# Kernel tuning notes

Hardware: AMD Instinct MI355X
Metric: run time of the kernel (lower is better)

The kernel has to match this reference:

```python
import jax, jax.numpy as jnp
import numpy as np

D_MODEL = 1024
NUM_HEADS = 16
HEAD_DIM = D_MODEL // NUM_HEADS  # 64
# NOTE: the original module passes scale=attention_head_size, so scores are
# MULTIPLIED by head_dim (64), not divided by sqrt(head_dim). Faithful quirk.
SCALE = float(HEAD_DIM)


def setup_inputs() -> dict:
    key = jax.random.key(0)
    ks = jax.random.split(key, 6)
    bs, s, d = 2, 2048, D_MODEL
    q = jax.random.normal(ks[0], (bs, s, d), dtype=jnp.float32)
    k = jax.random.normal(ks[1], (bs, s, d), dtype=jnp.float32)
    v = jax.random.normal(ks[2], (bs, s, d), dtype=jnp.float32)
    # nn.Linear weights, shape (out, in); no bias (qkv_bias=False)
    init = 1.0 / np.sqrt(d)
    Wq = jax.random.uniform(ks[3], (d, d), jnp.float32, -init, init)
    Wk = jax.random.uniform(ks[4], (d, d), jnp.float32, -init, init)
    Wv = jax.random.uniform(ks[5], (d, d), jnp.float32, -init, init)
    return {"q": q, "k": k, "v": v, "Wq": Wq, "Wk": Wk, "Wv": Wv}


def _split_heads(x):
    bs, s, _ = x.shape
    return x.reshape(bs, s, NUM_HEADS, HEAD_DIM).transpose(0, 2, 1, 3)  # bhsd


def reference(q, k, v, Wq, Wk, Wv):
    bs, s, d = q.shape
    qh = _split_heads(q @ Wq.T)  # [b,h,s,hd]
    kh = _split_heads(k @ Wk.T)
    vh = _split_heads(v @ Wv.T)
    sims = jnp.einsum('bhqd,bhkd->bhqk', qh, kh) * SCALE
    attn = jax.nn.softmax(sims, axis=-1)
    out = jnp.einsum('bhqk,bhkd->bhqd', attn, vh)  # [b,h,s,hd]
    out = out.transpose(0, 2, 1, 3).reshape(bs, s, d)
    return out
```

## Files before the change

### kernel.cpp

```cpp
#include <hip/hip_runtime.h>


typedef _Float16 half4 __attribute__((ext_vector_type(4)));
typedef _Float16 half8 __attribute__((ext_vector_type(8)));
typedef float floatx4 __attribute__((ext_vector_type(4)));

#define MFMA_F16(a, b, c) __builtin_amdgcn_mfma_f32_16x16x32_f16((a), (b), (c), 0, 0, 0)

constexpr int SEQ = 2048;
constexpr int DM = 1024;
constexpr int NH = 16;
constexpr int HD = 64;
constexpr float QSCALE = 92.33248261689366f;

__device__ __forceinline__ void gl2lds16(const _Float16* g, _Float16* l) {
  __builtin_amdgcn_global_load_lds(
      (const __attribute__((address_space(1))) void*)g,
      (__attribute__((address_space(3))) void*)l, 16, 0, 0);
}

__device__ inline void split4(const float4 f, half4& h, half4& l) {
  h[0] = (_Float16)f.x; l[0] = (_Float16)(f.x - (float)h[0]);
  h[1] = (_Float16)f.y; l[1] = (_Float16)(f.y - (float)h[1]);
  h[2] = (_Float16)f.z; l[2] = (_Float16)(f.z - (float)h[2]);
  h[3] = (_Float16)f.w; l[3] = (_Float16)(f.w - (float)h[3]);
}

__global__ __launch_bounds__(256) void convert_all(
    const float* __restrict__ q, const float* __restrict__ k,
    const float* __restrict__ v, const float* __restrict__ Wq,
    const float* __restrict__ Wk, const float* __restrict__ Wv,
    _Float16* __restrict__ xq_h, _Float16* __restrict__ xq_l,
    _Float16* __restrict__ xk_h, _Float16* __restrict__ xk_l,
    _Float16* __restrict__ xv_h,
    _Float16* __restrict__ Wqh, _Float16* __restrict__ Wql,
    _Float16* __restrict__ Wkh, _Float16* __restrict__ Wkl,
    _Float16* __restrict__ Wvh)
{
  const int bid = blockIdx.x;
  const float* src; _Float16* dh; _Float16* dl; int do_lo, i0;
  if (bid < 4096)       { src = q;  dh = xq_h; dl = xq_l; do_lo = 1; i0 = bid; }
  else if (bid < 8192)  { src = k;  dh = xk_h; dl = xk_l; do_lo = 1; i0 = bid - 4096; }
  else if (bid < 12288) { src = v;  dh = xv_h; dl = xv_h; do_lo = 0; i0 = bid - 8192; }
  else if (bid < 13312) { src = Wq; dh = Wqh;  dl = Wql;  do_lo = 1; i0 = bid - 12288; }
  else if (bid < 14336) { src = Wk; dh = Wkh;  dl = Wkl;  do_lo = 1; i0 = bid - 13312; }
  else                  { src = Wv; dh = Wvh;  dl = Wvh;  do_lo = 0; i0 = bid - 14336; }
  const int idx = i0 * 256 + threadIdx.x;
  float4 f = ((const float4*)src)[idx];
  half4 h, l; split4(f, h, l);
  *(half4*)(dh + (size_t)idx * 4) = h;
  if (do_lo) *(half4*)(dl + (size_t)idx * 4) = l;
}

__global__ __launch_bounds__(256, 1) void proj3_kernel(
    const _Float16* __restrict__ xq_h, const _Float16* __restrict__ xq_l,
    const _Float16* __restrict__ xk_h, const _Float16* __restrict__ xk_l,
    const _Float16* __restrict__ xv_h,
    const _Float16* __restrict__ Wqh, const _Float16* __restrict__ Wql,
    const _Float16* __restrict__ Wkh, const _Float16* __restrict__ Wkl,
    const _Float16* __restrict__ Wvh,
    _Float16* __restrict__ qh_hi, _Float16* __restrict__ qh_lo,
    _Float16* __restrict__ kh_hi, _Float16* __restrict__ kh_lo,
    _Float16* __restrict__ vh)
{
  __shared__ __align__(16) _Float16 Ahs[128][64];
  __shared__ __align__(16) _Float16 Als[128][64];
  __shared__ __align__(16) _Float16 Bhs[128][64];
  __shared__ __align__(16) _Float16 Bls[128][64];

  const int z = blockIdx.z;
  const _Float16 *Ahg, *Alg, *Bhg, *Blg;
  _Float16 *yh, *yl;
  float scale; int three;
  if (z == 0)      { Ahg = xq_h; Alg = xq_l; Bhg = Wqh; Blg = Wql;
                     yh = qh_hi; yl = qh_lo; scale = QSCALE; three = 1; }
  else if (z == 1) { Ahg = xk_h; Alg = xk_l; Bhg = Wkh; Blg = Wkl;
                     yh = kh_hi; yl = kh_lo; scale = 1.0f; three = 1; }
  else             { Ahg = xv_h; Alg = xv_h; Bhg = Wvh; Blg = Wvh;
                     yh = vh;    yl = vh;    scale = 1.0f; three = 0; }

  const int tid = threadIdx.x;
  const int bm = blockIdx.x;
  const int bn = blockIdx.y;
  const int lane = tid & 63, l15 = lane & 15, quad = lane >> 4;
  const int w = tid >> 6, wm = w >> 1, wn = w & 1;

  const int r8 = lane >> 3;
  const int cp8 = (((lane & 7) ^ r8)) * 8;
  int grow[4]; _Float16* la[4]; _Float16* lal[4]; _Float16* lb[4]; _Float16* lbl[4];
  #pragma unroll
  for (int i = 0; i < 4; i++) {
    const int g = w * 4 + i;
    grow[i] = g * 8 + r8;
    la[i]  = &Ahs[0][0] + g * 512;
    lal[i] = &Als[0][0] + g * 512;
    lb[i]  = &Bhs[0][0] + g * 512;
    lbl[i] = &Bls[0][0] + g * 512;
  }

  floatx4 acc[4][4];
  #pragma unroll
  for (int mt = 0; mt < 4; mt++)
    #pragma unroll
    for (int nt = 0; nt < 4; nt++)
      acc[mt][nt] = (floatx4){0.f, 0.f, 0.f, 0.f};

  for (int kk = 0; kk < DM; kk += 64) {
    __syncthreads();
    #pragma unroll
    for (int i = 0; i < 4; i++) {
      const size_t ga = (size_t)(bm * 128 + grow[i]) * DM + kk + cp8;
      const size_t gb = (size_t)(bn * 128 + grow[i]) * DM + kk + cp8;
      gl2lds16(Ahg + ga, la[i]);
      gl2lds16(Bhg + gb, lb[i]);
      if (three) {
        gl2lds16(Alg + ga, lal[i]);
        gl2lds16(Blg + gb, lbl[i]);
      }
    }
    __syncthreads();

    #pragma unroll
    for (int kc = 0; kc < 2; kc++) {
      const int swz = ((kc * 4 + quad) ^ (l15 & 7)) * 8;
      half8 ah[4], bh_[4], al[4], bl[4];
      #pragma unroll
      for (int t = 0; t < 4; t++) {
        ah[t]  = *(const half8*)&Ahs[wm * 64 + t * 16 + l15][swz];
        bh_[t] = *(const half8*)&Bhs[wn * 64 + t * 16 + l15][swz];
        if (three) {
          al[t] = *(const half8*)&Als[wm * 64 + t * 16 + l15][swz];
          bl[t] = *(const half8*)&Bls[wn * 64 + t * 16 + l15][swz];
        }
      }
      if (three) {
        #pragma unroll
        for (int mt = 0; mt < 4; mt++)
          #pragma unroll
          for (int nt = 0; nt < 4; nt++) {
            floatx4 t0 = MFMA_F16(ah[mt], bh_[nt], acc[mt][nt]);
            t0 = MFMA_F16(ah[mt], bl[nt], t0);
            acc[mt][nt] = MFMA_F16(al[mt], bh_[nt], t0);
          }
      } else {
        #pragma unroll
        for (int mt = 0; mt < 4; mt++)
          #pragma unroll
          for (int nt = 0; nt < 4; nt++)
            acc[mt][nt] = MFMA_F16(ah[mt], bh_[nt], acc[mt][nt]);
      }
    }
  }

  #pragma unroll
  for (int mt = 0; mt < 4; mt++)
    #pragma unroll
    for (int nt = 0; nt < 4; nt++)
      #pragma unroll
      for (int r = 0; r < 4; r++) {
        int gm = bm * 128 + wm * 64 + mt * 16 + quad * 4 + r;
        int gn = bn * 128 + wn * 64 + nt * 16 + l15;
        int b = gm >> 11, s = gm & 2047;
        int h = gn >> 6, d = gn & 63;
        size_t idx = ((size_t)(b * NH + h) * SEQ + s) * HD + d;
        float val = acc[mt][nt][r] * scale;
        _Float16 hi = (_Float16)val;
        yh[idx] = hi;
        if (three) yl[idx] = (_Float16)(val - (float)hi);
      }
}

__global__ __launch_bounds__(256) void transpose_v(const _Float16* __restrict__ vh,
                                                   _Float16* __restrict__ vhT)
{
  __shared__ __align__(16) _Float16 T[128][72];
  const int bh = blockIdx.x, sc = blockIdx.y, tid = threadIdx.x;
  const _Float16* src = vh + ((size_t)bh * SEQ + sc * 128) * HD;
  #pragma unroll
  for (int i = 0; i < 4; i++) {
    int c = i * 256 + tid, row = c >> 3, off = (c & 7) * 8;
    *(half8*)&T[row][off] = *(const half8*)(src + (size_t)row * HD + off);
  }
  __syncthreads();
  _Float16* dst = vhT + (size_t)bh * HD * SEQ + sc * 128;
  #pragma unroll
  for (int i = 0; i < 4; i++) {
    int c = i * 256 + tid, hd = c >> 4, off = (c & 15) * 8;
    int base32 = off & ~31, qsel = (off >> 3) & 3;
    half8 vv;
    #pragma unroll
    for (int j = 0; j < 8; j++) {
      int s_local = base32 + 16 * (j >> 2) + 4 * qsel + (j & 3);
      vv[j] = T[s_local][hd];
    }
    *(half8*)(dst + (size_t)hd * SEQ + off) = vv;
  }
}

__global__ __launch_bounds__(256, 4) void flash_kernel(
    const _Float16* __restrict__ qh_hi, const _Float16* __restrict__ qh_lo,
    const _Float16* __restrict__ kh_hi, const _Float16* __restrict__ kh_lo,
    const _Float16* __restrict__ vhT, float* __restrict__ Op, float2* __restrict__ ml)
{
  __shared__ __align__(16) _Float16 Kh[2][64][64];
  __shared__ __align__(16) _Float16 Kl[2][64][64];
  __shared__ __align__(16) _Float16 Vt[64][64];

  const int id = blockIdx.x;
  const int seq_ = id >> 3;
  const int bh = (id & 7) + 8 * (seq_ & 3);
  const int rem = seq_ >> 2;
  const int qb = rem & 15;
  const int kh = rem >> 4;
  const int tid = threadIdx.x;
  const int wq = tid >> 6;
  const int lane = tid & 63, l15 = lane & 15, quad = lane >> 4;

  const size_t bh_off = (size_t)bh * SEQ * HD;
  const _Float16* __restrict__ kh_p = kh_hi + bh_off;
  const _Float16* __restrict__ kl_p = kh_lo + bh_off;
  const _Float16* __restrict__ vt_p = vhT + (size_t)bh * HD * SEQ;
  const int qrow0 = qb * 128 + wq * 32;

  half8 bqh[2][2], bql[2][2];
  #pragma unroll
  for (int g = 0; g < 2; g++) {
    const _Float16* qp_h = qh_hi + bh_off + (size_t)(qrow0 + g * 16 + l15) * HD;
    const _Float16* qp_l = qh_lo + bh_off + (size_t)(qrow0 + g * 16 + l15) * HD;
    #pragma unroll
    for (int kc = 0; kc < 2; kc++) {
      bqh[g][kc] = *(const half8*)(qp_h + kc * 32 + quad * 8);
      bql[g][kc] = *(const half8*)(qp_l + kc * 32 + quad * 8);
    }
  }

  const int r8 = lane >> 3;
  const int cp8 = ((lane & 7) ^ r8) * 8;

  float m_[2] = {-3.0e38f, -3.0e38f};
  float l_[2] = {0.f, 0.f};
  floatx4 Oacc[2][4];
  #pragma unroll
  for (int g = 0; g < 2; g++)
    #pragma unroll
    for (int nd = 0; nd < 4; nd++) Oacc[g][nd] = (floatx4){0.f, 0.f, 0.f, 0.f};

  const int kt0 = kh * 16;
  {
    const int kbase = kt0 * 64;
    #pragma unroll
    for (int i = 0; i < 2; i++) {
      const int g = wq * 2 + i;
      const int r = g * 8 + r8;
      gl2lds16(kh_p + (size_t)(kbase + r) * HD + cp8, &Kh[0][0][0] + g * 512);
      gl2lds16(kl_p + (size_t)(kbase + r) * HD + cp8, &Kl[0][0][0] + g * 512);
    }
  }

  for (int kt = kt0; kt < kt0 + 16; kt++) {
    const int cur = kt & 1;
    const int kbase = kt * 64;
    __syncthreads();

    #pragma unroll
    for (int i = 0; i < 2; i++) {
      const int g = wq * 2 + i;
      const int r = g * 8 + r8;
      gl2lds16(vt_p + (size_t)r * SEQ + kbase + cp8, &Vt[0][0] + g * 512);
    }
    if (kt + 1 < kt0 + 16) {
      const int kb2 = (kt + 1) * 64, nxt = cur ^ 1;
      #pragma unroll
      for (int i = 0; i < 2; i++) {
        const int g = wq * 2 + i;
        const int r = g * 8 + r8;
        gl2lds16(kh_p + (size_t)(kb2 + r) * HD + cp8, &Kh[nxt][0][0] + g * 512);
        gl2lds16(kl_p + (size_t)(kb2 + r) * HD + cp8, &Kl[nxt][0][0] + g * 512);
      }
    }

    floatx4 sacc[2][4];
    const int r7 = l15 & 7;
    __builtin_amdgcn_s_setprio(1);
    #pragma unroll
    for (int nt = 0; nt < 4; nt++) {
      half8 akh0 = *(const half8*)&Kh[cur][nt * 16 + l15][((0 * 4 + quad) ^ r7) * 8];
      half8 akh1 = *(const half8*)&Kh[cur][nt * 16 + l15][((1 * 4 + quad) ^ r7) * 8];
      half8 akl0 = *(const half8*)&Kl[cur][nt * 16 + l15][((0 * 4 + quad) ^ r7) * 8];
      half8 akl1 = *(const half8*)&Kl[cur][nt * 16 + l15][((1 * 4 + quad) ^ r7) * 8];
      #pragma unroll
      for (int g = 0; g < 2; g++) {
        floatx4 s4 = (floatx4){0.f, 0.f, 0.f, 0.f};
        s4 = MFMA_F16(akh0, bqh[g][0], s4);
        s4 = MFMA_F16(akh1, bqh[g][1], s4);
        s4 = MFMA_F16(akh0, bql[g][0], s4);
        s4 = MFMA_F16(akh1, bql[g][1], s4);
        s4 = MFMA_F16(akl0, bqh[g][0], s4);
        s4 = MFMA_F16(akl1, bqh[g][1], s4);
        sacc[g][nt] = s4;
      }
    }
    __builtin_amdgcn_s_setprio(0);

    float alpha2[2];
    half8 bp8g[2][2];
    #pragma unroll
    for (int g = 0; g < 2; g++) {
      float rmax = sacc[g][0][0];
      #pragma unroll
      for (int nt = 0; nt < 4; nt++)
        #pragma unroll
        for (int r = 0; r < 4; r++) rmax = fmaxf(rmax, sacc[g][nt][r]);
      rmax = fmaxf(rmax, __shfl_xor(rmax, 16, 64));
      rmax = fmaxf(rmax, __shfl_xor(rmax, 32, 64));
      const float mnew = fmaxf(m_[g], rmax);
      alpha2[g] = exp2f(m_[g] - mnew);
      m_[g] = mnew;

      float rsum = 0.f;
      #pragma unroll
      for (int nt = 0; nt < 4; nt++)
        #pragma unroll
        for (int r = 0; r < 4; r++) {
          float p = exp2f(sacc[g][nt][r] - mnew);
          sacc[g][nt][r] = p;
          rsum += p;
        }
      rsum += __shfl_xor(rsum, 16, 64);
      rsum += __shfl_xor(rsum, 32, 64);
      l_[g] = l_[g] * alpha2[g] + rsum;

      #pragma unroll
      for (int kc = 0; kc < 2; kc++)
        #pragma unroll
        for (int j = 0; j < 8; j++)
          bp8g[g][kc][j] = (_Float16)sacc[g][2 * kc + (j >> 2)][j & 3];
    }

    __syncthreads();

    half8 av[4][2];
    #pragma unroll
    for (int nd = 0; nd < 4; nd++) {
      av[nd][0] = *(const half8*)&Vt[nd * 16 + l15][((0 * 4 + quad) ^ r7) * 8];
      av[nd][1] = *(const half8*)&Vt[nd * 16 + l15][((1 * 4 + quad) ^ r7) * 8];
    }

    __builtin_amdgcn_s_setprio(1);
    #pragma unroll
    for (int g = 0; g < 2; g++) {
      #pragma unroll
      for (int nd = 0; nd < 4; nd++) {
        Oacc[g][nd][0] *= alpha2[g]; Oacc[g][nd][1] *= alpha2[g];
        Oacc[g][nd][2] *= alpha2[g]; Oacc[g][nd][3] *= alpha2[g];
        Oacc[g][nd] = MFMA_F16(av[nd][0], bp8g[g][0], Oacc[g][nd]);
        Oacc[g][nd] = MFMA_F16(av[nd][1], bp8g[g][1], Oacc[g][nd]);
      }
    }
    __builtin_amdgcn_s_setprio(0);
  }

  const size_t fqbase = (size_t)bh * SEQ + qrow0;
  #pragma unroll
  for (int g = 0; g < 2; g++) {
    const size_t fq = fqbase + g * 16 + l15;
    float* ob = Op + ((size_t)kh * 65536 + fq) * HD;
    #pragma unroll
    for (int nd = 0; nd < 4; nd++) {
      float4 vv;
      vv.x = Oacc[g][nd][0]; vv.y = Oacc[g][nd][1];
      vv.z = Oacc[g][nd][2]; vv.w = Oacc[g][nd][3];
      *(float4*)(ob + nd * 16 + quad * 4) = vv;
    }
    if (quad == 0) ml[kh * 65536 + fq] = make_float2(m_[g], l_[g]);
  }
}

__global__ __launch_bounds__(256) void merge_kernel(const float* __restrict__ Op,
                                                    const float2* __restrict__ ml,
                                                    float* __restrict__ out)
{
  const int tid = threadIdx.x;
  const int fq = blockIdx.x * 64 + (tid >> 2);
  const int dp = (tid & 3) * 16;
  float2 m0 = ml[fq], m1 = ml[65536 + fq];
  float M = fmaxf(m0.x, m1.x);
  float w0 = exp2f(m0.x - M), w1 = exp2f(m1.x - M);
  float rinv = 1.0f / (m0.y * w0 + m1.y * w1);
  int bh = fq >> 11, s = fq & 2047, b = bh >> 4, h = bh & 15;
  float* ob = out + ((size_t)(b * SEQ + s)) * DM + h * HD + dp;
  const float* p0 = Op + (size_t)fq * HD + dp;
  const float* p1 = p0 + (size_t)65536 * HD;
  #pragma unroll
  for (int j = 0; j < 4; j++) {
    float4 a = *(const float4*)(p0 + 4 * j);
    float4 c = *(const float4*)(p1 + 4 * j);
    float4 r;
    r.x = (a.x * w0 + c.x * w1) * rinv;
    r.y = (a.y * w0 + c.y * w1) * rinv;
    r.z = (a.z * w0 + c.z * w1) * rinv;
    r.w = (a.w * w0 + c.w * w1) * rinv;
    *(float4*)(ob + 4 * j) = r;
  }
}

extern "C" void kernel_launch(void* const* d_in, const int* in_sizes, int n_in,
                              void* d_out, int out_size, void* d_ws, size_t ws_size,
                              hipStream_t stream) {
  const float* q  = (const float*)d_in[0];
  const float* k  = (const float*)d_in[1];
  const float* v  = (const float*)d_in[2];
  const float* Wq = (const float*)d_in[3];
  const float* Wk = (const float*)d_in[4];
  const float* Wv = (const float*)d_in[5];
  float* out = (float*)d_out;

  char* W = (char*)d_ws;
  const size_t MiB = 1ull << 20;
  _Float16* qh_hi = (_Float16*)(W + 0 * MiB);
  _Float16* qh_lo = (_Float16*)(W + 8 * MiB);
  _Float16* kh_hi = (_Float16*)(W + 16 * MiB);
  _Float16* kh_lo = (_Float16*)(W + 24 * MiB);
  _Float16* vhT   = (_Float16*)(W + 32 * MiB);
  _Float16* vh    = (_Float16*)(W + 40 * MiB);
  _Float16* xq_h  = (_Float16*)(W + 48 * MiB);
  _Float16* xq_l  = (_Float16*)(W + 56 * MiB);
  _Float16* xk_h  = (_Float16*)(W + 64 * MiB);
  _Float16* xk_l  = (_Float16*)(W + 72 * MiB);
  _Float16* xv_h  = (_Float16*)(W + 80 * MiB);
  _Float16* Wqh   = (_Float16*)(W + 88 * MiB);
  _Float16* Wql   = (_Float16*)(W + 90 * MiB);
  _Float16* Wkh   = (_Float16*)(W + 92 * MiB);
  _Float16* Wkl   = (_Float16*)(W + 94 * MiB);
  _Float16* Wvh   = (_Float16*)(W + 96 * MiB);
  float*    Op    = (float*)  (W + 40 * MiB);
  float2*   mlp   = (float2*) (W + 98 * MiB);

  convert_all<<<15360, 256, 0, stream>>>(q, k, v, Wq, Wk, Wv,
                                         xq_h, xq_l, xk_h, xk_l, xv_h,
                                         Wqh, Wql, Wkh, Wkl, Wvh);
  proj3_kernel<<<dim3(32, 8, 3), 256, 0, stream>>>(
      xq_h, xq_l, xk_h, xk_l, xv_h, Wqh, Wql, Wkh, Wkl, Wvh,
      qh_hi, qh_lo, kh_hi, kh_lo, vh);
  transpose_v<<<dim3(32, 16), 256, 0, stream>>>(vh, vhT);
  flash_kernel<<<1024, 256, 0, stream>>>(qh_hi, qh_lo, kh_hi, kh_lo, vhT, Op, mlp);
  merge_kernel<<<1024, 256, 0, stream>>>(Op, mlp, out);
}
```

Measured before the change: 295.4 us.

## Fuse V transpose into projection epilogue and drop setprio hints in flash

The V projection epilogue now writes its fp16 output directly in the transposed, MFMA-permuted layout that the flash kernel expects. This removes the separate transpose_v kernel launch and its extra read and write of V. The flash kernel also loses its s_setprio hints around the MFMA blocks, which changes wave scheduling priority. The direct transposed stores are 8-byte half4 writes strided by SEQ, which may coalesce less well than the old epilogue's row-major writes.

New measurement: 286.6 us (median of 2 runs). 1.03x faster.

```diff
diff --git a/kernel.cpp b/kernel.cpp
--- a/kernel.cpp
+++ b/kernel.cpp
@@ -61,7 +61,7 @@
     const _Float16* __restrict__ Wvh,
     _Float16* __restrict__ qh_hi, _Float16* __restrict__ qh_lo,
     _Float16* __restrict__ kh_hi, _Float16* __restrict__ kh_lo,
-    _Float16* __restrict__ vh)
+    _Float16* __restrict__ vhT)
 {
   __shared__ __align__(16) _Float16 Ahs[128][64];
   __shared__ __align__(16) _Float16 Als[128][64];
@@ -77,7 +77,7 @@
   else if (z == 1) { Ahg = xk_h; Alg = xk_l; Bhg = Wkh; Blg = Wkl;
                      yh = kh_hi; yl = kh_lo; scale = 1.0f; three = 1; }
   else             { Ahg = xv_h; Alg = xv_h; Bhg = Wvh; Blg = Wvh;
-                     yh = vh;    yl = vh;    scale = 1.0f; three = 0; }
+                     yh = vhT;   yl = vhT;   scale = 1.0f; three = 0; }
 
   const int tid = threadIdx.x;
   const int bm = blockIdx.x;
@@ -152,48 +152,43 @@
     }
   }
 
-  #pragma unroll
-  for (int mt = 0; mt < 4; mt++)
-    #pragma unroll
-    for (int nt = 0; nt < 4; nt++)
-      #pragma unroll
-      for (int r = 0; r < 4; r++) {
-        int gm = bm * 128 + wm * 64 + mt * 16 + quad * 4 + r;
-        int gn = bn * 128 + wn * 64 + nt * 16 + l15;
-        int b = gm >> 11, s = gm & 2047;
-        int h = gn >> 6, d = gn & 63;
-        size_t idx = ((size_t)(b * NH + h) * SEQ + s) * HD + d;
-        float val = acc[mt][nt][r] * scale;
-        _Float16 hi = (_Float16)val;
-        yh[idx] = hi;
-        if (three) yl[idx] = (_Float16)(val - (float)hi);
-      }
-}
-
-__global__ __launch_bounds__(256) void transpose_v(const _Float16* __restrict__ vh,
-                                                   _Float16* __restrict__ vhT)
-{
-  __shared__ __align__(16) _Float16 T[128][72];
-  const int bh = blockIdx.x, sc = blockIdx.y, tid = threadIdx.x;
-  const _Float16* src = vh + ((size_t)bh * SEQ + sc * 128) * HD;
-  #pragma unroll
-  for (int i = 0; i < 4; i++) {
-    int c = i * 256 + tid, row = c >> 3, off = (c & 7) * 8;
-    *(half8*)&T[row][off] = *(const half8*)(src + (size_t)row * HD + off);
-  }
-  __syncthreads();
-  _Float16* dst = vhT + (size_t)bh * HD * SEQ + sc * 128;
-  #pragma unroll
-  for (int i = 0; i < 4; i++) {
-    int c = i * 256 + tid, hd = c >> 4, off = (c & 15) * 8;
-    int base32 = off & ~31, qsel = (off >> 3) & 3;
-    half8 vv;
-    #pragma unroll
-    for (int j = 0; j < 8; j++) {
-      int s_local = base32 + 16 * (j >> 2) + 4 * qsel + (j & 3);
-      vv[j] = T[s_local][hd];
-    }
-    *(half8*)(dst + (size_t)hd * SEQ + off) = vv;
+  if (three) {
+    #pragma unroll
+    for (int mt = 0; mt < 4; mt++)
+      #pragma unroll
+      for (int nt = 0; nt < 4; nt++)
+        #pragma unroll
+        for (int r = 0; r < 4; r++) {
+          int gm = bm * 128 + wm * 64 + mt * 16 + quad * 4 + r;
+          int gn = bn * 128 + wn * 64 + nt * 16 + l15;
+          int b = gm >> 11, s = gm & 2047;
+          int h = gn >> 6, d = gn & 63;
+          size_t idx = ((size_t)(b * NH + h) * SEQ + s) * HD + d;
+          float val = acc[mt][nt][r] * scale;
+          _Float16 hi = (_Float16)val;
+          yh[idx] = hi;
+          yl[idx] = (_Float16)(val - (float)hi);
+        }
+  } else {
+    const int b = bm >> 4;
+    const int h = bn * 2 + wn;
+    const int bh = b * NH + h;
+    const int sbase = (bm & 15) * 128 + wm * 64;
+    _Float16* vt = vhT + (size_t)bh * HD * SEQ;
+    #pragma unroll
+    for (int mt = 0; mt < 4; mt++) {
+      const int pos = sbase + (mt >> 1) * 32 + quad * 8 + (mt & 1) * 4;
+      #pragma unroll
+      for (int nt = 0; nt < 4; nt++) {
+        const int d = nt * 16 + l15;
+        half4 hv;
+        hv[0] = (_Float16)acc[mt][nt][0];
+        hv[1] = (_Float16)acc[mt][nt][1];
+        hv[2] = (_Float16)acc[mt][nt][2];
+        hv[3] = (_Float16)acc[mt][nt][3];
+        *(half4*)(vt + (size_t)d * SEQ + pos) = hv;
+      }
+    }
   }
 }
 
@@ -281,7 +276,6 @@
 
     floatx4 sacc[2][4];
     const int r7 = l15 & 7;
-    __builtin_amdgcn_s_setprio(1);
     #pragma unroll
     for (int nt = 0; nt < 4; nt++) {
       half8 akh0 = *(const half8*)&Kh[cur][nt * 16 + l15][((0 * 4 + quad) ^ r7) * 8];
@@ -300,7 +294,6 @@
         sacc[g][nt] = s4;
       }
     }
-    __builtin_amdgcn_s_setprio(0);
 
     float alpha2[2];
     half8 bp8g[2][2];
@@ -346,7 +339,6 @@
       av[nd][1] = *(const half8*)&Vt[nd * 16 + l15][((1 * 4 + quad) ^ r7) * 8];
     }
 
-    __builtin_amdgcn_s_setprio(1);
     #pragma unroll
     for (int g = 0; g < 2; g++) {
       #pragma unroll
@@ -357,7 +349,6 @@
         Oacc[g][nd] = MFMA_F16(av[nd][1], bp8g[g][1], Oacc[g][nd]);
       }
     }
-    __builtin_amdgcn_s_setprio(0);
   }
 
   const size_t fqbase = (size_t)bh * SEQ + qrow0;
@@ -422,7 +413,6 @@
   _Float16* kh_hi = (_Float16*)(W + 16 * MiB);
   _Float16* kh_lo = (_Float16*)(W + 24 * MiB);
   _Float16* vhT   = (_Float16*)(W + 32 * MiB);
-  _Float16* vh    = (_Float16*)(W + 40 * MiB);
   _Float16* xq_h  = (_Float16*)(W + 48 * MiB);
   _Float16* xq_l  = (_Float16*)(W + 56 * MiB);
   _Float16* xk_h  = (_Float16*)(W + 64 * MiB);
@@ -441,8 +431,7 @@
                                          Wqh, Wql, Wkh, Wkl, Wvh);
   proj3_kernel<<<dim3(32, 8, 3), 256, 0, stream>>>(
       xq_h, xq_l, xk_h, xk_l, xv_h, Wqh, Wql, Wkh, Wkl, Wvh,
-      qh_hi, qh_lo, kh_hi, kh_lo, vh);
-  transpose_v<<<dim3(32, 16), 256, 0, stream>>>(vh, vhT);
+      qh_hi, qh_lo, kh_hi, kh_lo, vhT);
   flash_kernel<<<1024, 256, 0, stream>>>(qh_hi, qh_lo, kh_hi, kh_lo, vhT, Op, mlp);
   merge_kernel<<<1024, 256, 0, stream>>>(Op, mlp, out);
 }
```
